# Kernel tuning notes

Measured on AMD Instinct MI355X. Metric: run time of the kernel, lower is better.

## Reference

```python
import jax, jax.numpy as jnp
import numpy as np

PC_RANGE = (-50.0, -50.0, -4.0, 50.0, 50.0, 4.0)
IMG_H, IMG_W = 256.0, 704.0
EPS = 1e-5


def _bilinear_sample(feat, u, v):
    # feat [H,W,C]; u,v [M] in [0,1]; matches F.grid_sample(align_corners=False, padding_mode='zeros')
    H, W, _ = feat.shape
    x = u * W - 0.5
    y = v * H - 0.5
    x0 = jnp.floor(x)
    y0 = jnp.floor(y)
    dx = (x - x0)[:, None]
    dy = (y - y0)[:, None]
    x0 = x0.astype(jnp.int32)
    y0 = y0.astype(jnp.int32)

    def g(xi, yi):
        inb = ((xi >= 0) & (xi < W) & (yi >= 0) & (yi < H)).astype(feat.dtype)[:, None]
        return feat[jnp.clip(yi, 0, H - 1), jnp.clip(xi, 0, W - 1)] * inb

    return (g(x0, y0) * (1 - dx) * (1 - dy) + g(x0 + 1, y0) * dx * (1 - dy)
            + g(x0, y0 + 1) * (1 - dx) * dy + g(x0 + 1, y0 + 1) * dx * dy)


def _conv1x1(t, w, b):
    return jnp.einsum('bchw,oc->bohw', t, w) + b[None, :, None, None]


def _inorm(t, eps=1e-5):
    # InstanceNorm2d (affine=False): normalize per (b, c) over spatial dims
    m = t.mean(axis=(2, 3), keepdims=True)
    var = t.var(axis=(2, 3), keepdims=True)
    return (t - m) * jax.lax.rsqrt(var + eps)


def _forward(feat, lidar2img, bev_pos, pe_w1, pe_b1, pe_w2, pe_b2, pe_w3, pe_b3,
             c1_w, c1_b, c2_w, c2_b, c3_w, c3_b):
    B, N, C, Hf, Wf = feat.shape
    _, P, Hb, Wb, _ = bev_pos.shape
    Q = Hb * Wb
    lo = jnp.asarray(PC_RANGE[:3], feat.dtype)
    hi = jnp.asarray(PC_RANGE[3:], feat.dtype)
    # 'b p h w d -> b (h w) p d', then scale normalized coords into pc_range
    ref01 = jnp.transpose(bev_pos, (0, 2, 3, 1, 4)).reshape(B, Q, P, 3)
    ref = ref01 * (hi - lo) + lo
    # project through per-camera lidar2img (homogeneous)
    pts = jnp.concatenate([ref, jnp.ones_like(ref[..., :1])], axis=-1)  # [B,Q,P,4]
    cam = jnp.einsum('bnij,bqpj->bnqpi', lidar2img, pts)                # [B,N,Q,P,4]
    homo = cam[..., 2]
    z = jnp.maximum(homo, EPS)
    u = cam[..., 0] / z / IMG_W
    v = cam[..., 1] / z / IMG_H
    valid = ((homo > EPS) & (u > 0.0) & (u < 1.0) & (v > 0.0) & (v < 1.0)).astype(feat.dtype)
    # bilinear gather per camera; feats to channel-last ('b n (g c) h w -> (b g) n h w c', G=1)
    fmap = jnp.transpose(feat, (0, 1, 3, 4, 2)).reshape(B * N, Hf, Wf, C)
    samp = jax.vmap(_bilinear_sample)(fmap, u.reshape(B * N, Q * P), v.reshape(B * N, Q * P))
    samp = samp.reshape(B, N, Q, P, C) * valid[..., None]
    samp = samp.sum(axis=1)  # sum over cameras -> [B,Q,P,C]
    # PositionalEncodingMap(3 -> 256 -> 256 -> 128) on normalized reference points
    pe = jax.nn.relu(ref01 @ pe_w1 + pe_b1)
    pe = jax.nn.relu(pe @ pe_w2 + pe_b2)
    pe = pe @ pe_w3 + pe_b3
    samp = samp + pe
    # 'b (h w) g p c -> b (p g c) h w' with g=1
    x = jnp.transpose(samp.reshape(B, Hb, Wb, P, C), (0, 3, 4, 1, 2)).reshape(B, P * C, Hb, Wb)
    gelu = lambda t: jax.nn.gelu(t, approximate=False)
    x = gelu(_inorm(_conv1x1(x, c1_w, c1_b)))
    x = gelu(_inorm(_conv1x1(x, c2_w, c2_b)))
    x = _conv1x1(x, c3_w, c3_b)
    return x


def setup_inputs() -> dict:
    key = jax.random.key(0)
    ks = jax.random.split(key, 16)
    B, N, C, Hf, Wf = 1, 6, 128, 32, 88
    P, Hb, Wb = 4, 160, 160
    E = 128
    MID = 256
    s = 0.02
    return {
        'feat': jax.random.normal(ks[0], (B, N, C, Hf, Wf), jnp.float32),
        'lidar2img': jax.random.normal(ks[1], (B, N, 4, 4), jnp.float32),
        'bev_pos': jax.random.uniform(ks[2], (B, P, Hb, Wb, 3), jnp.float32),
        'pe_w1': jax.random.normal(ks[3], (3, MID), jnp.float32) * s,
        'pe_b1': jnp.zeros((MID,), jnp.float32),
        'pe_w2': jax.random.normal(ks[4], (MID, MID), jnp.float32) * s,
        'pe_b2': jnp.zeros((MID,), jnp.float32),
        'pe_w3': jax.random.normal(ks[5], (MID, E), jnp.float32) * s,
        'pe_b3': jnp.zeros((E,), jnp.float32),
        'c1_w': jax.random.normal(ks[6], (4 * E, P * 128), jnp.float32) * s,
        'c1_b': jnp.zeros((4 * E,), jnp.float32),
        'c2_w': jax.random.normal(ks[7], (E, 4 * E), jnp.float32) * s,
        'c2_b': jnp.zeros((E,), jnp.float32),
        'c3_w': jax.random.normal(ks[8], (E, E), jnp.float32) * s,
        'c3_b': jnp.zeros((E,), jnp.float32),
    }


def reference(feat, lidar2img, bev_pos, pe_w1, pe_b1, pe_w2, pe_b2, pe_w3, pe_b3,
              c1_w, c1_b, c2_w, c2_b, c3_w, c3_b):
    return _forward(feat, lidar2img, bev_pos, pe_w1, pe_b1, pe_w2, pe_b2, pe_w3, pe_b3,
                    c1_w, c1_b, c2_w, c2_b, c3_w, c3_b)
```

## Files before the change

kernel.cpp:

```cpp
#include <hip/hip_runtime.h>
#include <cstdint>
#include <cstddef>

using frag8 = __attribute__((ext_vector_type(8))) short;
using f32x4 = __attribute__((ext_vector_type(4))) float;

__device__ __forceinline__ float b2f_bits(unsigned short u) {
    union { uint32_t u32; float f; } x; x.u32 = ((uint32_t)u) << 16; return x.f;
}
__device__ __forceinline__ float b2f_lo(uint32_t pk) {
    return __builtin_bit_cast(float, pk << 16);
}
__device__ __forceinline__ float b2f_hi(uint32_t pk) {
    return __builtin_bit_cast(float, pk & 0xffff0000u);
}
__device__ __forceinline__ unsigned short f2b(float f) {
    uint32_t u = __builtin_bit_cast(uint32_t, f);
    uint32_t r = (u + 0x7fffu + ((u >> 16) & 1u)) >> 16;
    return (unsigned short)r;
}
__device__ __forceinline__ uint32_t cvtpk_bf16(float lo, float hi) {
    uint32_t r;
    asm("v_cvt_pk_bf16_f32 %0, %1, %2" : "=v"(r) : "v"(lo), "v"(hi));
    return r;
}

#define HF 32
#define WFEAT 88
#define NCAM 6
#define NPT 102400
#define BM 128
#define BN 128
#define BK 64

__global__ __launch_bounds__(256) void k_prep(const float* __restrict__ feat,
                                              const float* __restrict__ pw2,
                                              const float* __restrict__ pw3,
                                              const float* __restrict__ c1w,
                                              const float* __restrict__ c2w,
                                              const float* __restrict__ c3w,
                                              const float* __restrict__ l2i,
                                              const float* __restrict__ bev,
                                              unsigned short* __restrict__ featT,
                                              unsigned short* __restrict__ W2Tb,
                                              unsigned short* __restrict__ W3Tb,
                                              unsigned short* __restrict__ C1Wb,
                                              unsigned short* __restrict__ C2Wb,
                                              unsigned short* __restrict__ C3Wb,
                                              float* __restrict__ stats,
                                              int* __restrict__ poff,
                                              float4* __restrict__ pwts) {
    __shared__ unsigned short tile[64 * 132];
    int b = blockIdx.x, t = threadIdx.x;
    if (b < 2400) {
        int idx = b * 256 + t;
        int n = idx / NPT, pt = idx - n * NPT;
        int q = pt >> 2, p = pt & 3;
        int h = q / 160, w = q - h * 160;
        const float* bv = bev + ((p * 160 + h) * 160 + w) * 3;
        float rx = bv[0] * 100.f - 50.f;
        float ry = bv[1] * 100.f - 50.f;
        float rz = bv[2] * 8.f - 4.f;
        const float* M = l2i + n * 16;
        float c0   = M[0] * rx + M[1] * ry + M[2]  * rz + M[3];
        float c1v  = M[4] * rx + M[5] * ry + M[6]  * rz + M[7];
        float homo = M[8] * rx + M[9] * ry + M[10] * rz + M[11];
        float z = fmaxf(homo, 1e-5f);
        float u = c0 / z / 704.0f;
        float v = c1v / z / 256.0f;
        if (!(homo > 1e-5f && u > 0.f && u < 1.f && v > 0.f && v < 1.f)) {
            poff[idx] = -1;
            return;
        }
        float fx = u * (float)WFEAT - 0.5f;
        float fy = v * (float)HF - 0.5f;
        float fx0 = floorf(fx), fy0 = floorf(fy);
        float dx = fx - fx0, dy = fy - fy0;
        int x0 = (int)fx0, y0 = (int)fy0;
        float wxa = (x0 < 0) ? dx : 1.f - dx;
        float wxb = (x0 >= 0 && x0 < WFEAT - 1) ? dx : 0.f;
        float wya = (y0 < 0) ? dy : 1.f - dy;
        float wyb = (y0 >= 0 && y0 < HF - 1) ? dy : 0.f;
        int bx = max(x0, 0), by = max(y0, 0);
        poff[idx] = ((n * HF + by) * WFEAT + bx) << 7;
        pwts[idx] = make_float4(wxa * wya, wxb * wya, wxa * wyb, wxb * wyb);
        return;
    }
    b -= 2400;
    if (b < 264) {
        int n = b / 44;
        int s0 = (b - n * 44) * 64;
        #pragma unroll
        for (int i = 0; i < 32; ++i) {
            int e = i * 256 + t;
            int c = e >> 6, sl = e & 63;
            tile[sl * 132 + c] = f2b(feat[(size_t)(n * 128 + c) * 2816 + s0 + sl]);
        }
        __syncthreads();
        #pragma unroll
        for (int j = 0; j < 8; ++j) {
            int flat = j * 1024 + t * 4;
            int sl = flat >> 7, c = flat & 127;
            ushort4 v = *(const ushort4*)(tile + sl * 132 + c);
            *(ushort4*)(featT + (size_t)(n * 2816 + s0 + sl) * 128 + c) = v;
        }
        return;
    }
    b -= 264;
    if (b < 256) {
        int idx = b * 256 + t;
        int r = idx >> 8, c = idx & 255;
        W2Tb[c * 256 + r] = f2b(pw2[idx]);
        return;
    }
    b -= 256;
    if (b < 128) {
        int idx = b * 256 + t;
        int r = idx >> 7, c = idx & 127;
        W3Tb[c * 256 + r] = f2b(pw3[idx]);
        return;
    }
    b -= 128;
    if (b < 1024) { int idx = b * 256 + t; C1Wb[idx] = f2b(c1w[idx]); return; }
    b -= 1024;
    if (b < 256)  { int idx = b * 256 + t; C2Wb[idx] = f2b(c2w[idx]); return; }
    b -= 256;
    if (b < 64)   { int idx = b * 256 + t; C3Wb[idx] = f2b(c3w[idx]); return; }
    #pragma unroll
    for (int j = 0; j < 10; ++j) stats[t * 10 + j] = 0.f;
}

__global__ __launch_bounds__(256) void k_sample2(const unsigned short* __restrict__ featT,
                                                 const int* __restrict__ poff,
                                                 const float4* __restrict__ pwts,
                                                 unsigned short* __restrict__ samp) {
    int pt = blockIdx.x * 4 + (threadIdx.x >> 6);
    int lane = threadIdx.x & 63;
    int c2 = lane * 2;
    int offs[NCAM];
    float4 ww[NCAM];
    #pragma unroll
    for (int n = 0; n < NCAM; ++n) offs[n] = poff[n * NPT + pt];
    #pragma unroll
    for (int n = 0; n < NCAM; ++n) ww[n] = pwts[n * NPT + pt];
    float acc0 = 0.f, acc1 = 0.f;
    #pragma unroll
    for (int n = 0; n < NCAM; ++n) {
        if (offs[n] >= 0) {
            const unsigned short* base = featT + offs[n] + c2;
            uint32_t p00 = *(const uint32_t*)(base);
            uint32_t p01 = *(const uint32_t*)(base + 128);
            uint32_t p10 = *(const uint32_t*)(base + WFEAT * 128);
            uint32_t p11 = *(const uint32_t*)(base + WFEAT * 128 + 128);
            float4 w = ww[n];
            acc0 += w.x * b2f_lo(p00) + w.y * b2f_lo(p01) + w.z * b2f_lo(p10) + w.w * b2f_lo(p11);
            acc1 += w.x * b2f_hi(p00) + w.y * b2f_hi(p01) + w.z * b2f_hi(p10) + w.w * b2f_hi(p11);
        }
    }
    uint32_t outpk = (uint32_t)f2b(acc0) | ((uint32_t)f2b(acc1) << 16);
    *(uint32_t*)(samp + (size_t)pt * 128 + c2) = outpk;
}

__device__ __forceinline__ void stage_tile(const unsigned short* __restrict__ g, int ld,
                                           unsigned short* lds, int wave, int lane) {
    #pragma unroll
    for (int j = 0; j < 4; ++j) {
        int idx = wave * 256 + j * 64 + lane;
        int r = idx >> 3;
        int cs = idx & 7;
        int cl = cs ^ (r & 7);
        __builtin_amdgcn_global_load_lds(
            (const __attribute__((address_space(1))) void*)(g + (size_t)r * ld + cl * 8),
            (__attribute__((address_space(3))) void*)(lds + wave * 2048 + j * 512),
            16, 0, 0);
    }
}

__device__ __forceinline__ frag8 frag_read(const unsigned short* lds, int row, int chunk) {
    return *(const frag8*)(lds + row * 64 + ((chunk ^ (row & 7)) << 3));
}

__device__ __forceinline__ void mma_tile(const unsigned short* As, const unsigned short* Bs,
                                         int wm, int wn, int lane, f32x4 (&acc)[4][4]) {
    int lm = lane & 15, lq = lane >> 4;
    #pragma unroll
    for (int kk = 0; kk < 2; ++kk) {
        frag8 a[4], b[4];
        #pragma unroll
        for (int t = 0; t < 4; ++t) a[t] = frag_read(As, wm * 64 + t * 16 + lm, kk * 4 + lq);
        #pragma unroll
        for (int t = 0; t < 4; ++t) b[t] = frag_read(Bs, wn * 64 + t * 16 + lm, kk * 4 + lq);
        #pragma unroll
        for (int tm = 0; tm < 4; ++tm)
            #pragma unroll
            for (int tn = 0; tn < 4; ++tn)
                acc[tm][tn] = __builtin_amdgcn_mfma_f32_16x16x32_bf16(a[tm], b[tn], acc[tm][tn], 0, 0, 0);
    }
}

template <int KT>
__device__ __forceinline__ void gemm_loop_pipe(const unsigned short* __restrict__ A, int ldA,
                                               const unsigned short* __restrict__ B, int ldB,
                                               unsigned short (*As)[BM * BK],
                                               unsigned short (*Bs)[BN * BK],
                                               int wave, int lane, int wm, int wn,
                                               f32x4 (&acc)[4][4]) {
    stage_tile(A, ldA, As[0], wave, lane);
    stage_tile(B, ldB, Bs[0], wave, lane);
    if (KT > 1) {
        stage_tile(A + BK, ldA, As[1], wave, lane);
        stage_tile(B + BK, ldB, Bs[1], wave, lane);
    }
    #pragma unroll
    for (int kt = 0; kt < KT; ++kt) {
        int cur = kt & 1;
        if (kt + 1 < KT) asm volatile("s_waitcnt vmcnt(8)" ::: "memory");
        else             asm volatile("s_waitcnt vmcnt(0)" ::: "memory");
        __builtin_amdgcn_s_barrier();
        mma_tile(As[cur], Bs[cur], wm, wn, lane, acc);
        asm volatile("s_waitcnt lgkmcnt(0)" ::: "memory");
        __builtin_amdgcn_s_barrier();
        if (kt + 2 < KT) {
            stage_tile(A + (kt + 2) * BK, ldA, As[cur], wave, lane);
            stage_tile(B + (kt + 2) * BK, ldB, Bs[cur], wave, lane);
        }
    }
}

__device__ __forceinline__ void build_h1_2(const float* __restrict__ wls, float x, float y, float z,
                                           int r, int c0, int kt, unsigned short* __restrict__ As) {
    #pragma unroll
    for (int j = 0; j < 2; ++j) {
        int cl = c0 + j;
        const float* wp = wls + kt * 64 + cl * 8;
        float4 a0l = *(const float4*)(wp),       a0h = *(const float4*)(wp + 4);
        float4 a1l = *(const float4*)(wp + 256), a1h = *(const float4*)(wp + 260);
        float4 a2l = *(const float4*)(wp + 512), a2h = *(const float4*)(wp + 516);
        float4 bbl = *(const float4*)(wp + 768), bbh = *(const float4*)(wp + 772);
        float v0 = fmaxf(x * a0l.x + y * a1l.x + z * a2l.x + bbl.x, 0.f);
        float v1 = fmaxf(x * a0l.y + y * a1l.y + z * a2l.y + bbl.y, 0.f);
        float v2 = fmaxf(x * a0l.z + y * a1l.z + z * a2l.z + bbl.z, 0.f);
        float v3 = fmaxf(x * a0l.w + y * a1l.w + z * a2l.w + bbl.w, 0.f);
        float v4 = fmaxf(x * a0h.x + y * a1h.x + z * a2h.x + bbh.x, 0.f);
        float v5 = fmaxf(x * a0h.y + y * a1h.y + z * a2h.y + bbh.y, 0.f);
        float v6 = fmaxf(x * a0h.z + y * a1h.z + z * a2h.z + bbh.z, 0.f);
        float v7 = fmaxf(x * a0h.w + y * a1h.w + z * a2h.w + bbh.w, 0.f);
        uint32_t q0 = cvtpk_bf16(v0, v1), q1 = cvtpk_bf16(v2, v3);
        uint32_t q2 = cvtpk_bf16(v4, v5), q3 = cvtpk_bf16(v6, v7);
        *(uint4*)(As + r * 64 + ((cl ^ (r & 7)) << 3)) = make_uint4(q0, q1, q2, q3);
    }
}

__global__ __launch_bounds__(256) void k_pe12(const float* __restrict__ bev,
                                              const float* __restrict__ pw1,
                                              const float* __restrict__ pb1,
                                              const unsigned short* __restrict__ Bt,
                                              const float* __restrict__ bias,
                                              unsigned short* __restrict__ H2) {
    __shared__ unsigned short As[64 * BK];
    __shared__ unsigned short Bs[2][256 * BK];
    __shared__ __align__(16) float wls[4 * 256];
    __shared__ float bevs[3 * 64];
    int t = threadIdx.x, lane = t & 63, wave = t >> 6;
    int m0 = blockIdx.x * 64;
    {
        int i = t * 4;
        int j = i >> 8, c = i & 255;
        float4 v = (j < 3) ? *(const float4*)(pw1 + j * 256 + c)
                           : *(const float4*)(pb1 + c);
        *(float4*)(wls + i) = v;
    }
    if (t < 64) {
        int m = m0 + t;
        int q = m >> 2, p = m & 3;
        int h = q / 160, w = q - h * 160;
        const float* bv = bev + ((size_t)((p * 160 + h) * 160 + w)) * 3;
        bevs[t] = bv[0]; bevs[64 + t] = bv[1]; bevs[128 + t] = bv[2];
    }
    __syncthreads();
    int r = t & 63;
    int c0 = (t >> 6) * 2;
    float x = bevs[r], y = bevs[64 + r], z = bevs[128 + r];
    int lm = lane & 15, lq = lane >> 4;
    f32x4 acc[4][4] = {};
    stage_tile(Bt, 256, Bs[0], wave, lane);
    stage_tile(Bt + 128 * 256, 256, Bs[0] + 8192, wave, lane);
    stage_tile(Bt + BK, 256, Bs[1], wave, lane);
    stage_tile(Bt + 128 * 256 + BK, 256, Bs[1] + 8192, wave, lane);
    #pragma unroll
    for (int kt = 0; kt < 4; ++kt) {
        int cur = kt & 1;
        build_h1_2(wls, x, y, z, r, c0, kt, As);
        asm volatile("s_waitcnt lgkmcnt(0)" ::: "memory");
        if (kt + 1 < 4) asm volatile("s_waitcnt vmcnt(8)" ::: "memory");
        else            asm volatile("s_waitcnt vmcnt(0)" ::: "memory");
        __builtin_amdgcn_s_barrier();
        #pragma unroll
        for (int kk = 0; kk < 2; ++kk) {
            int ch = kk * 4 + lq;
            frag8 a[4], b[4];
            #pragma unroll
            for (int tt = 0; tt < 4; ++tt) a[tt] = frag_read(As, tt * 16 + lm, ch);
            #pragma unroll
            for (int tn = 0; tn < 4; ++tn) b[tn] = frag_read(Bs[cur], wave * 64 + tn * 16 + lm, ch);
            #pragma unroll
            for (int tm = 0; tm < 4; ++tm)
                #pragma unroll
                for (int tn = 0; tn < 4; ++tn)
                    acc[tm][tn] = __builtin_amdgcn_mfma_f32_16x16x32_bf16(a[tm], b[tn], acc[tm][tn], 0, 0, 0);
        }
        asm volatile("s_waitcnt lgkmcnt(0)" ::: "memory");
        __builtin_amdgcn_s_barrier();
        if (kt + 2 < 4) {
            stage_tile(Bt + (kt + 2) * BK, 256, Bs[cur], wave, lane);
            stage_tile(Bt + 128 * 256 + (kt + 2) * BK, 256, Bs[cur] + 8192, wave, lane);
        }
    }
    #pragma unroll
    for (int tn = 0; tn < 4; ++tn) {
        int n = wave * 64 + tn * 16 + lm;
        float bn = bias[n];
        #pragma unroll
        for (int tm = 0; tm < 4; ++tm) {
            int mb = m0 + tm * 16 + lq * 4;
            #pragma unroll
            for (int rr = 0; rr < 4; ++rr)
                H2[(size_t)(mb + rr) * 256 + n] = f2b(fmaxf(acc[tm][tn][rr] + bn, 0.f));
        }
    }
}

__global__ __launch_bounds__(256) void k_gemm_pe3(const unsigned short* __restrict__ A,
                                                  const unsigned short* __restrict__ Bt,
                                                  const float* __restrict__ bias,
                                                  const unsigned short* __restrict__ samp,
                                                  unsigned short* __restrict__ X) {
    __shared__ unsigned short As[2][BM * BK], Bs[2][BN * BK];
    int lane = threadIdx.x & 63, wave = threadIdx.x >> 6;
    int wm = wave >> 1, wn = wave & 1;
    int m0 = blockIdx.x * BM;
    f32x4 acc[4][4] = {};
    gemm_loop_pipe<4>(A + (size_t)m0 * 256, 256, Bt, 256, As, Bs, wave, lane, wm, wn, acc);
    int lm = lane & 15, lq = lane >> 4;
    #pragma unroll
    for (int tn = 0; tn < 4; ++tn) {
        int n = wn * 64 + tn * 16 + lm;
        float bn = bias[n];
        #pragma unroll
        for (int tm = 0; tm < 4; ++tm) {
            int mb = m0 + wm * 64 + tm * 16 + lq * 4;
            #pragma unroll
            for (int rr = 0; rr < 4; ++rr) {
                size_t off = (size_t)(mb + rr) * 128 + n;
                X[off] = f2b(acc[tm][tn][rr] + bn + b2f_bits(samp[off]));
            }
        }
    }
}

template <int K, bool STATS>
__global__ __launch_bounds__(256) void k_gemm_conv(const unsigned short* __restrict__ A,
                                                   const unsigned short* __restrict__ Bt,
                                                   const float* __restrict__ bias,
                                                   unsigned short* __restrict__ Y, int ldY,
                                                   float* __restrict__ st, int C) {
    __shared__ unsigned short As[2][BM * BK], Bs[2][BN * BK];
    int lane = threadIdx.x & 63, wave = threadIdx.x >> 6;
    int wm = wave >> 1, wn = wave & 1;
    int m0 = blockIdx.x * BM, n0 = blockIdx.y * BN;
    f32x4 acc[4][4] = {};
    gemm_loop_pipe<K / BK>(A + (size_t)m0 * K, K, Bt + (size_t)n0 * K, K,
                           As, Bs, wave, lane, wm, wn, acc);
    int lm = lane & 15, lq = lane >> 4;
    #pragma unroll
    for (int tn = 0; tn < 4; ++tn) {
        int n = n0 + wn * 64 + tn * 16 + lm;
        float bn = bias[n];
        float s1 = 0.f, s2 = 0.f;
        #pragma unroll
        for (int tm = 0; tm < 4; ++tm) {
            int mb = m0 + wm * 64 + tm * 16 + lq * 4;
            #pragma unroll
            for (int rr = 0; rr < 4; ++rr) {
                float v = acc[tm][tn][rr] + bn;
                Y[(size_t)(mb + rr) * ldY + n] = f2b(v);
                if (STATS) { s1 += v; s2 += v * v; }
            }
        }
        if (STATS) {
            s1 += __shfl_xor(s1, 16); s1 += __shfl_xor(s1, 32);
            s2 += __shfl_xor(s2, 16); s2 += __shfl_xor(s2, 32);
            if (lq == 0) { atomicAdd(&st[n], s1); atomicAdd(&st[C + n], s2); }
        }
    }
}

__global__ __launch_bounds__(256) void k_gemm_conv3(const unsigned short* __restrict__ A,
                                                    const unsigned short* __restrict__ Bt,
                                                    const float* __restrict__ bias,
                                                    float* __restrict__ out) {
    __shared__ unsigned short As[2][BM * BK], Bs[2][BN * BK];
    int lane = threadIdx.x & 63, wave = threadIdx.x >> 6;
    int wm = wave >> 1, wn = wave & 1;
    int m0 = blockIdx.x * BM;
    f32x4 acc[4][4] = {};
    gemm_loop_pipe<2>(A + (size_t)m0 * 128, 128, Bt, 128, As, Bs, wave, lane, wm, wn, acc);
    int lm = lane & 15, lq = lane >> 4;
    #pragma unroll
    for (int tn = 0; tn < 4; ++tn) {
        int n = wn * 64 + tn * 16 + lm;
        float bn = bias[n];
        #pragma unroll
        for (int tm = 0; tm < 4; ++tm) {
            int mb = m0 + wm * 64 + tm * 16 + lq * 4;
            float4 pk;
            pk.x = acc[tm][tn][0] + bn;
            pk.y = acc[tm][tn][1] + bn;
            pk.z = acc[tm][tn][2] + bn;
            pk.w = acc[tm][tn][3] + bn;
            *(float4*)(out + (size_t)n * 25600 + mb) = pk;
        }
    }
}

__global__ void k_normgelu8f(const unsigned short* __restrict__ Y, const float* __restrict__ st,
                             unsigned short* __restrict__ X2, int Cmask, int C, float inv_n,
                             int total8) {
    int i8 = blockIdx.x * 256 + threadIdx.x;
    if (i8 >= total8) return;
    int e0 = i8 * 8;
    int c = e0 & Cmask;
    uint4 y = *(const uint4*)(Y + e0);
    float4 s1a = *(const float4*)(st + c);
    float4 s1b = *(const float4*)(st + c + 4);
    float4 s2a = *(const float4*)(st + C + c);
    float4 s2b = *(const float4*)(st + C + c + 4);
    float mu[8] = { s1a.x * inv_n, s1a.y * inv_n, s1a.z * inv_n, s1a.w * inv_n,
                    s1b.x * inv_n, s1b.y * inv_n, s1b.z * inv_n, s1b.w * inv_n };
    float sq[8] = { s2a.x, s2a.y, s2a.z, s2a.w, s2b.x, s2b.y, s2b.z, s2b.w };
    float rs[8];
    #pragma unroll
    for (int j = 0; j < 8; ++j) rs[j] = rsqrtf(sq[j] * inv_n - mu[j] * mu[j] + 1e-5f);
    const float is2 = 0.70710678118654752f;
    unsigned int yw[4] = {y.x, y.y, y.z, y.w};
    unsigned int ow[4];
    #pragma unroll
    for (int j = 0; j < 4; ++j) {
        float v0 = (b2f_bits((unsigned short)(yw[j] & 0xffffu)) - mu[j * 2]) * rs[j * 2];
        float v1 = (b2f_bits((unsigned short)(yw[j] >> 16)) - mu[j * 2 + 1]) * rs[j * 2 + 1];
        float g0 = 0.5f * v0 * (1.f + erff(v0 * is2));
        float g1 = 0.5f * v1 * (1.f + erff(v1 * is2));
        ow[j] = (uint32_t)f2b(g0) | ((uint32_t)f2b(g1) << 16);
    }
    *(uint4*)(X2 + e0) = make_uint4(ow[0], ow[1], ow[2], ow[3]);
}

extern "C" void kernel_launch(void* const* d_in, const int* in_sizes, int n_in,
                              void* d_out, int out_size, void* d_ws, size_t ws_size,
                              hipStream_t stream) {
    (void)in_sizes; (void)n_in; (void)out_size; (void)ws_size;
    const float* feat = (const float*)d_in[0];
    const float* l2i  = (const float*)d_in[1];
    const float* bev  = (const float*)d_in[2];
    const float* pw1  = (const float*)d_in[3];
    const float* pb1  = (const float*)d_in[4];
    const float* pw2  = (const float*)d_in[5];
    const float* pb2  = (const float*)d_in[6];
    const float* pw3  = (const float*)d_in[7];
    const float* pb3  = (const float*)d_in[8];
    const float* c1w  = (const float*)d_in[9];
    const float* c1b  = (const float*)d_in[10];
    const float* c2w  = (const float*)d_in[11];
    const float* c2b  = (const float*)d_in[12];
    const float* c3w  = (const float*)d_in[13];
    const float* c3b  = (const float*)d_in[14];
    float* outp = (float*)d_out;
    char* ws = (char*)d_ws;

    unsigned short* featT = (unsigned short*)(ws + 0);
    unsigned short* W2Tb  = (unsigned short*)(ws + 4348416);
    unsigned short* W3Tb  = (unsigned short*)(ws + 4479488);
    unsigned short* C1Wb  = (unsigned short*)(ws + 4545024);
    unsigned short* C2Wb  = (unsigned short*)(ws + 5069312);
    unsigned short* C3Wb  = (unsigned short*)(ws + 5200384);
    float* stats          = (float*)(ws + 5233152);
    int*    poff          = (int*)(ws + 5247488);
    float4* pwts          = (float4*)(ws + 7705088);
    char* BUF1 = ws + 17535488;
    char* BUF2 = ws + 69964288;
    char* BUF3 = ws + 122393088;

    float* st512 = stats;
    float* st128 = stats + 2048;

    unsigned short* H2   = (unsigned short*)BUF2;
    unsigned short* samp = (unsigned short*)BUF3;
    unsigned short* X    = (unsigned short*)BUF1;
    unsigned short* Y1   = (unsigned short*)BUF2;
    unsigned short* X2   = (unsigned short*)BUF3;
    unsigned short* Y2   = (unsigned short*)BUF1;
    unsigned short* X3   = (unsigned short*)(BUF1 + 6553600);

    k_prep<<<4393, 256, 0, stream>>>(feat, pw2, pw3, c1w, c2w, c3w, l2i, bev,
                                     featT, W2Tb, W3Tb, C1Wb, C2Wb, C3Wb, stats,
                                     poff, pwts);

    k_sample2<<<25600, 256, 0, stream>>>(featT, poff, pwts, samp);

    k_pe12<<<1600, 256, 0, stream>>>(bev, pw1, pb1, W2Tb, pb2, H2);
    k_gemm_pe3<<<dim3(800, 1), 256, 0, stream>>>(H2, W3Tb, pb3, samp, X);

    k_gemm_conv<512, true><<<dim3(200, 4), 256, 0, stream>>>(X, C1Wb, c1b, Y1, 512, st512, 512);
    k_normgelu8f<<<6400, 256, 0, stream>>>(Y1, st512, X2, 511, 512, 1.f / 25600.f, 1638400);

    k_gemm_conv<512, true><<<dim3(200, 1), 256, 0, stream>>>(X2, C2Wb, c2b, Y2, 128, st128, 128);
    k_normgelu8f<<<1600, 256, 0, stream>>>(Y2, st128, X3, 127, 128, 1.f / 25600.f, 409600);

    k_gemm_conv3<<<200, 256, 0, stream>>>(X3, C3Wb, c3b, outp);
}
```

Before: 263.0 us.

## Fuse projection into sampler and fuse PE MLP layers 2 and 3

Result: slower. 292.9 us (+11.4%).

```diff
diff --git a/kernel.cpp b/kernel.cpp
--- a/kernel.cpp
+++ b/kernel.cpp
@@ -39,28 +39,74 @@
                                               const float* __restrict__ c1w,
                                               const float* __restrict__ c2w,
                                               const float* __restrict__ c3w,
-                                              const float* __restrict__ l2i,
-                                              const float* __restrict__ bev,
                                               unsigned short* __restrict__ featT,
                                               unsigned short* __restrict__ W2Tb,
                                               unsigned short* __restrict__ W3Tb,
                                               unsigned short* __restrict__ C1Wb,
                                               unsigned short* __restrict__ C2Wb,
                                               unsigned short* __restrict__ C3Wb,
-                                              float* __restrict__ stats,
-                                              int* __restrict__ poff,
-                                              float4* __restrict__ pwts) {
+                                              float* __restrict__ stats) {
     __shared__ unsigned short tile[64 * 132];
     int b = blockIdx.x, t = threadIdx.x;
-    if (b < 2400) {
+    if (b < 264) {
+        int n = b / 44;
+        int s0 = (b - n * 44) * 64;
+        #pragma unroll
+        for (int i = 0; i < 32; ++i) {
+            int e = i * 256 + t;
+            int c = e >> 6, sl = e & 63;
+            tile[sl * 132 + c] = f2b(feat[(size_t)(n * 128 + c) * 2816 + s0 + sl]);
+        }
+        __syncthreads();
+        #pragma unroll
+        for (int j = 0; j < 8; ++j) {
+            int flat = j * 1024 + t * 4;
+            int sl = flat >> 7, c = flat & 127;
+            ushort4 v = *(const ushort4*)(tile + sl * 132 + c);
+            *(ushort4*)(featT + (size_t)(n * 2816 + s0 + sl) * 128 + c) = v;
+        }
+        return;
+    }
+    b -= 264;
+    if (b < 256) {
         int idx = b * 256 + t;
-        int n = idx / NPT, pt = idx - n * NPT;
-        int q = pt >> 2, p = pt & 3;
-        int h = q / 160, w = q - h * 160;
-        const float* bv = bev + ((p * 160 + h) * 160 + w) * 3;
-        float rx = bv[0] * 100.f - 50.f;
-        float ry = bv[1] * 100.f - 50.f;
-        float rz = bv[2] * 8.f - 4.f;
+        int r = idx >> 8, c = idx & 255;
+        W2Tb[c * 256 + r] = f2b(pw2[idx]);
+        return;
+    }
+    b -= 256;
+    if (b < 128) {
+        int idx = b * 256 + t;
+        int r = idx >> 7, c = idx & 127;
+        W3Tb[c * 256 + r] = f2b(pw3[idx]);
+        return;
+    }
+    b -= 128;
+    if (b < 1024) { int idx = b * 256 + t; C1Wb[idx] = f2b(c1w[idx]); return; }
+    b -= 1024;
+    if (b < 256)  { int idx = b * 256 + t; C2Wb[idx] = f2b(c2w[idx]); return; }
+    b -= 256;
+    if (b < 64)   { int idx = b * 256 + t; C3Wb[idx] = f2b(c3w[idx]); return; }
+    #pragma unroll
+    for (int j = 0; j < 10; ++j) stats[t * 10 + j] = 0.f;
+}
+
+__global__ __launch_bounds__(256) void k_sample2(const unsigned short* __restrict__ featT,
+                                                 const float* __restrict__ l2i,
+                                                 const float* __restrict__ bev,
+                                                 unsigned short* __restrict__ samp) {
+    int pt = blockIdx.x * 4 + (threadIdx.x >> 6);
+    int lane = threadIdx.x & 63;
+    int c2 = lane * 2;
+    int q = pt >> 2, p = pt & 3;
+    int h = q / 160, w = q - h * 160;
+    const float* bv = bev + ((p * 160 + h) * 160 + w) * 3;
+    float rx = bv[0] * 100.f - 50.f;
+    float ry = bv[1] * 100.f - 50.f;
+    float rz = bv[2] * 8.f - 4.f;
+    float acc0 = 0.f, acc1 = 0.f;
+    #pragma unroll
+    for (int n = 0; n < NCAM; ++n) {
         const float* M = l2i + n * 16;
         float c0   = M[0] * rx + M[1] * ry + M[2]  * rz + M[3];
         float c1v  = M[4] * rx + M[5] * ry + M[6]  * rz + M[7];
@@ -68,93 +114,25 @@
         float z = fmaxf(homo, 1e-5f);
         float u = c0 / z / 704.0f;
         float v = c1v / z / 256.0f;
-        if (!(homo > 1e-5f && u > 0.f && u < 1.f && v > 0.f && v < 1.f)) {
-            poff[idx] = -1;
-            return;
-        }
-        float fx = u * (float)WFEAT - 0.5f;
-        float fy = v * (float)HF - 0.5f;
-        float fx0 = floorf(fx), fy0 = floorf(fy);
-        float dx = fx - fx0, dy = fy - fy0;
-        int x0 = (int)fx0, y0 = (int)fy0;
-        float wxa = (x0 < 0) ? dx : 1.f - dx;
-        float wxb = (x0 >= 0 && x0 < WFEAT - 1) ? dx : 0.f;
-        float wya = (y0 < 0) ? dy : 1.f - dy;
-        float wyb = (y0 >= 0 && y0 < HF - 1) ? dy : 0.f;
-        int bx = max(x0, 0), by = max(y0, 0);
-        poff[idx] = ((n * HF + by) * WFEAT + bx) << 7;
-        pwts[idx] = make_float4(wxa * wya, wxb * wya, wxa * wyb, wxb * wyb);
-        return;
-    }
-    b -= 2400;
-    if (b < 264) {
-        int n = b / 44;
-        int s0 = (b - n * 44) * 64;
-        #pragma unroll
-        for (int i = 0; i < 32; ++i) {
-            int e = i * 256 + t;
-            int c = e >> 6, sl = e & 63;
-            tile[sl * 132 + c] = f2b(feat[(size_t)(n * 128 + c) * 2816 + s0 + sl]);
-        }
-        __syncthreads();
-        #pragma unroll
-        for (int j = 0; j < 8; ++j) {
-            int flat = j * 1024 + t * 4;
-            int sl = flat >> 7, c = flat & 127;
-            ushort4 v = *(const ushort4*)(tile + sl * 132 + c);
-            *(ushort4*)(featT + (size_t)(n * 2816 + s0 + sl) * 128 + c) = v;
-        }
-        return;
-    }
-    b -= 264;
-    if (b < 256) {
-        int idx = b * 256 + t;
-        int r = idx >> 8, c = idx & 255;
-        W2Tb[c * 256 + r] = f2b(pw2[idx]);
-        return;
-    }
-    b -= 256;
-    if (b < 128) {
-        int idx = b * 256 + t;
-        int r = idx >> 7, c = idx & 127;
-        W3Tb[c * 256 + r] = f2b(pw3[idx]);
-        return;
-    }
-    b -= 128;
-    if (b < 1024) { int idx = b * 256 + t; C1Wb[idx] = f2b(c1w[idx]); return; }
-    b -= 1024;
-    if (b < 256)  { int idx = b * 256 + t; C2Wb[idx] = f2b(c2w[idx]); return; }
-    b -= 256;
-    if (b < 64)   { int idx = b * 256 + t; C3Wb[idx] = f2b(c3w[idx]); return; }
-    #pragma unroll
-    for (int j = 0; j < 10; ++j) stats[t * 10 + j] = 0.f;
-}
-
-__global__ __launch_bounds__(256) void k_sample2(const unsigned short* __restrict__ featT,
-                                                 const int* __restrict__ poff,
-                                                 const float4* __restrict__ pwts,
-                                                 unsigned short* __restrict__ samp) {
-    int pt = blockIdx.x * 4 + (threadIdx.x >> 6);
-    int lane = threadIdx.x & 63;
-    int c2 = lane * 2;
-    int offs[NCAM];
-    float4 ww[NCAM];
-    #pragma unroll
-    for (int n = 0; n < NCAM; ++n) offs[n] = poff[n * NPT + pt];
-    #pragma unroll
-    for (int n = 0; n < NCAM; ++n) ww[n] = pwts[n * NPT + pt];
-    float acc0 = 0.f, acc1 = 0.f;
-    #pragma unroll
-    for (int n = 0; n < NCAM; ++n) {
-        if (offs[n] >= 0) {
-            const unsigned short* base = featT + offs[n] + c2;
+        if (homo > 1e-5f && u > 0.f && u < 1.f && v > 0.f && v < 1.f) {
+            float fx = u * (float)WFEAT - 0.5f;
+            float fy = v * (float)HF - 0.5f;
+            float fx0 = floorf(fx), fy0 = floorf(fy);
+            float dx = fx - fx0, dy = fy - fy0;
+            int x0 = (int)fx0, y0 = (int)fy0;
+            float wxa = (x0 < 0) ? dx : 1.f - dx;
+            float wxb = (x0 >= 0 && x0 < WFEAT - 1) ? dx : 0.f;
+            float wya = (y0 < 0) ? dy : 1.f - dy;
+            float wyb = (y0 >= 0 && y0 < HF - 1) ? dy : 0.f;
+            int bx = max(x0, 0), by = max(y0, 0);
+            const unsigned short* base = featT + (((n * HF + by) * WFEAT + bx) << 7) + c2;
             uint32_t p00 = *(const uint32_t*)(base);
             uint32_t p01 = *(const uint32_t*)(base + 128);
             uint32_t p10 = *(const uint32_t*)(base + WFEAT * 128);
             uint32_t p11 = *(const uint32_t*)(base + WFEAT * 128 + 128);
-            float4 w = ww[n];
-            acc0 += w.x * b2f_lo(p00) + w.y * b2f_lo(p01) + w.z * b2f_lo(p10) + w.w * b2f_lo(p11);
-            acc1 += w.x * b2f_hi(p00) + w.y * b2f_hi(p01) + w.z * b2f_hi(p10) + w.w * b2f_hi(p11);
+            float w00 = wxa * wya, w01 = wxb * wya, w10 = wxa * wyb, w11 = wxb * wyb;
+            acc0 += w00 * b2f_lo(p00) + w01 * b2f_lo(p01) + w10 * b2f_lo(p10) + w11 * b2f_lo(p11);
+            acc1 += w00 * b2f_hi(p00) + w01 * b2f_hi(p01) + w10 * b2f_hi(p10) + w11 * b2f_hi(p11);
         }
     }
     uint32_t outpk = (uint32_t)f2b(acc0) | ((uint32_t)f2b(acc1) << 16);
@@ -251,16 +229,21 @@
     }
 }
 
-__global__ __launch_bounds__(256) void k_pe12(const float* __restrict__ bev,
-                                              const float* __restrict__ pw1,
-                                              const float* __restrict__ pb1,
-                                              const unsigned short* __restrict__ Bt,
-                                              const float* __restrict__ bias,
-                                              unsigned short* __restrict__ H2) {
-    __shared__ unsigned short As[64 * BK];
-    __shared__ unsigned short Bs[2][256 * BK];
-    __shared__ __align__(16) float wls[4 * 256];
-    __shared__ float bevs[3 * 64];
+__global__ __launch_bounds__(256) void k_pe123(const float* __restrict__ bev,
+                                               const float* __restrict__ pw1,
+                                               const float* __restrict__ pb1,
+                                               const unsigned short* __restrict__ W2t,
+                                               const float* __restrict__ pb2,
+                                               const unsigned short* __restrict__ W3t,
+                                               const float* __restrict__ pb3,
+                                               const unsigned short* __restrict__ samp,
+                                               unsigned short* __restrict__ X) {
+    __shared__ __align__(16) char smem[78592];
+    unsigned short* As  = (unsigned short*)smem;
+    unsigned short* Bs0 = (unsigned short*)(smem + 8192);
+    unsigned short* Bs1 = (unsigned short*)(smem + 40960);
+    float* wls  = (float*)(smem + 73728);
+    float* bevs = (float*)(smem + 77824);
     int t = threadIdx.x, lane = t & 63, wave = t >> 6;
     int m0 = blockIdx.x * 64;
     {
@@ -283,13 +266,13 @@
     float x = bevs[r], y = bevs[64 + r], z = bevs[128 + r];
     int lm = lane & 15, lq = lane >> 4;
     f32x4 acc[4][4] = {};
-    stage_tile(Bt, 256, Bs[0], wave, lane);
-    stage_tile(Bt + 128 * 256, 256, Bs[0] + 8192, wave, lane);
-    stage_tile(Bt + BK, 256, Bs[1], wave, lane);
-    stage_tile(Bt + 128 * 256 + BK, 256, Bs[1] + 8192, wave, lane);
+    stage_tile(W2t, 256, Bs0, wave, lane);
+    stage_tile(W2t + 128 * 256, 256, Bs0 + 8192, wave, lane);
+    stage_tile(W2t + BK, 256, Bs1, wave, lane);
+    stage_tile(W2t + 128 * 256 + BK, 256, Bs1 + 8192, wave, lane);
     #pragma unroll
     for (int kt = 0; kt < 4; ++kt) {
-        int cur = kt & 1;
+        unsigned short* Bcur = (kt & 1) ? Bs1 : Bs0;
         build_h1_2(wls, x, y, z, r, c0, kt, As);
         asm volatile("s_waitcnt lgkmcnt(0)" ::: "memory");
         if (kt + 1 < 4) asm volatile("s_waitcnt vmcnt(8)" ::: "memory");
@@ -302,7 +285,7 @@
             #pragma unroll
             for (int tt = 0; tt < 4; ++tt) a[tt] = frag_read(As, tt * 16 + lm, ch);
             #pragma unroll
-            for (int tn = 0; tn < 4; ++tn) b[tn] = frag_read(Bs[cur], wave * 64 + tn * 16 + lm, ch);
+            for (int tn = 0; tn < 4; ++tn) b[tn] = frag_read(Bcur, wave * 64 + tn * 16 + lm, ch);
             #pragma unroll
             for (int tm = 0; tm < 4; ++tm)
                 #pragma unroll
@@ -312,47 +295,64 @@
         asm volatile("s_waitcnt lgkmcnt(0)" ::: "memory");
         __builtin_amdgcn_s_barrier();
         if (kt + 2 < 4) {
-            stage_tile(Bt + (kt + 2) * BK, 256, Bs[cur], wave, lane);
-            stage_tile(Bt + 128 * 256 + (kt + 2) * BK, 256, Bs[cur] + 8192, wave, lane);
-        }
-    }
+            stage_tile(W2t + (kt + 2) * BK, 256, Bcur, wave, lane);
+            stage_tile(W2t + 128 * 256 + (kt + 2) * BK, 256, Bcur + 8192, wave, lane);
+        }
+    }
+    frag8 bw[4][2][2];
+    #pragma unroll
+    for (int kt = 0; kt < 4; ++kt)
+        #pragma unroll
+        for (int kk = 0; kk < 2; ++kk)
+            #pragma unroll
+            for (int tn = 0; tn < 2; ++tn) {
+                int n2 = wave * 32 + tn * 16 + lm;
+                bw[kt][kk][tn] = *(const frag8*)(W3t + (size_t)n2 * 256 + kt * 64 + (kk * 4 + lq) * 8);
+            }
+    unsigned short* H2s = Bs0;
     #pragma unroll
     for (int tn = 0; tn < 4; ++tn) {
-        int n = wave * 64 + tn * 16 + lm;
-        float bn = bias[n];
+        int c = tn * 16 + lm;
+        int nn = wave * 64 + c;
+        float bn = pb2[nn];
+        int chw = c >> 3, e = c & 7;
+        #pragma unroll
+        for (int tm = 0; tm < 4; ++tm)
+            #pragma unroll
+            for (int rr = 0; rr < 4; ++rr) {
+                int row = tm * 16 + lq * 4 + rr;
+                H2s[wave * 4096 + row * 64 + ((chw ^ (row & 7)) << 3) + e] =
+                    f2b(fmaxf(acc[tm][tn][rr] + bn, 0.f));
+            }
+    }
+    asm volatile("s_waitcnt lgkmcnt(0)" ::: "memory");
+    __builtin_amdgcn_s_barrier();
+    f32x4 acc2[4][2] = {};
+    #pragma unroll
+    for (int kt = 0; kt < 4; ++kt)
+        #pragma unroll
+        for (int kk = 0; kk < 2; ++kk) {
+            int ch = kk * 4 + lq;
+            frag8 a[4];
+            #pragma unroll
+            for (int tm = 0; tm < 4; ++tm) a[tm] = frag_read(H2s + kt * 4096, tm * 16 + lm, ch);
+            #pragma unroll
+            for (int tm = 0; tm < 4; ++tm)
+                #pragma unroll
+                for (int tn = 0; tn < 2; ++tn)
+                    acc2[tm][tn] = __builtin_amdgcn_mfma_f32_16x16x32_bf16(a[tm], bw[kt][kk][tn], acc2[tm][tn], 0, 0, 0);
+        }
+    #pragma unroll
+    for (int tn = 0; tn < 2; ++tn) {
+        int n2 = wave * 32 + tn * 16 + lm;
+        float bn = pb3[n2];
         #pragma unroll
         for (int tm = 0; tm < 4; ++tm) {
             int mb = m0 + tm * 16 + lq * 4;
             #pragma unroll
-            for (int rr = 0; rr < 4; ++rr)
-                H2[(size_t)(mb + rr) * 256 + n] = f2b(fmaxf(acc[tm][tn][rr] + bn, 0.f));
-        }
-    }
-}
-
-__global__ __launch_bounds__(256) void k_gemm_pe3(const unsigned short* __restrict__ A,
-                                                  const unsigned short* __restrict__ Bt,
-                                                  const float* __restrict__ bias,
-                                                  const unsigned short* __restrict__ samp,
-                                                  unsigned short* __restrict__ X) {
-    __shared__ unsigned short As[2][BM * BK], Bs[2][BN * BK];
-    int lane = threadIdx.x & 63, wave = threadIdx.x >> 6;
-    int wm = wave >> 1, wn = wave & 1;
-    int m0 = blockIdx.x * BM;
-    f32x4 acc[4][4] = {};
-    gemm_loop_pipe<4>(A + (size_t)m0 * 256, 256, Bt, 256, As, Bs, wave, lane, wm, wn, acc);
-    int lm = lane & 15, lq = lane >> 4;
-    #pragma unroll
-    for (int tn = 0; tn < 4; ++tn) {
-        int n = wn * 64 + tn * 16 + lm;
-        float bn = bias[n];
-        #pragma unroll
-        for (int tm = 0; tm < 4; ++tm) {
-            int mb = m0 + wm * 64 + tm * 16 + lq * 4;
-            #pragma unroll
             for (int rr = 0; rr < 4; ++rr) {
-                size_t off = (size_t)(mb + rr) * 128 + n;
-                X[off] = f2b(acc[tm][tn][rr] + bn + b2f_bits(samp[off]));
+                size_t off = (size_t)(mb + rr) * 128 + n2;
+                X[off] = f2b(acc2[tm][tn][rr] + bn + b2f_bits(samp[off]));
             }
         }
     }
@@ -484,8 +484,6 @@
     unsigned short* C2Wb  = (unsigned short*)(ws + 5069312);
     unsigned short* C3Wb  = (unsigned short*)(ws + 5200384);
     float* stats          = (float*)(ws + 5233152);
-    int*    poff          = (int*)(ws + 5247488);
-    float4* pwts          = (float4*)(ws + 7705088);
     char* BUF1 = ws + 17535488;
     char* BUF2 = ws + 69964288;
     char* BUF3 = ws + 122393088;
@@ -493,7 +491,6 @@
     float* st512 = stats;
     float* st128 = stats + 2048;
 
-    unsigned short* H2   = (unsigned short*)BUF2;
     unsigned short* samp = (unsigned short*)BUF3;
     unsigned short* X    = (unsigned short*)BUF1;
     unsigned short* Y1   = (unsigned short*)BUF2;
@@ -501,14 +498,12 @@
     unsigned short* Y2   = (unsigned short*)BUF1;
     unsigned short* X3   = (unsigned short*)(BUF1 + 6553600);
 
-    k_prep<<<4393, 256, 0, stream>>>(feat, pw2, pw3, c1w, c2w, c3w, l2i, bev,
-                                     featT, W2Tb, W3Tb, C1Wb, C2Wb, C3Wb, stats,
-                                     poff, pwts);
-
-    k_sample2<<<25600, 256, 0, stream>>>(featT, poff, pwts, samp);
-
-    k_pe12<<<1600, 256, 0, stream>>>(bev, pw1, pb1, W2Tb, pb2, H2);
-    k_gemm_pe3<<<dim3(800, 1), 256, 0, stream>>>(H2, W3Tb, pb3, samp, X);
+    k_prep<<<1993, 256, 0, stream>>>(feat, pw2, pw3, c1w, c2w, c3w,
+                                     featT, W2Tb, W3Tb, C1Wb, C2Wb, C3Wb, stats);
+
+    k_sample2<<<25600, 256, 0, stream>>>(featT, l2i, bev, samp);
+
+    k_pe123<<<1600, 256, 0, stream>>>(bev, pw1, pb1, W2Tb, pb2, W3Tb, pb3, samp, X);
 
     k_gemm_conv<512, true><<<dim3(200, 4), 256, 0, stream>>>(X, C1Wb, c1b, Y1, 512, st512, 512);
     k_normgelu8f<<<6400, 256, 0, stream>>>(Y1, st512, X2, 511, 512, 1.f / 25600.f, 1638400);
```
